# Kernel tuning notes

Hardware: AMD Instinct MI355X
Metric: run time of the kernel (lower is better)

## Reference

```python
import jax, jax.numpy as jnp
import numpy as np

D_MODEL = 1024
N_HEADS = 16
D_K = D_MODEL // N_HEADS
LN_EPS = 1e-5


def setup_inputs() -> dict:
    key = jax.random.key(0)
    ks = jax.random.split(key, 12)
    B, S, D = 4, 2048, D_MODEL
    s = 1.0 / np.sqrt(D)
    return {
        "Q": jax.random.normal(ks[0], (B, S, D), jnp.float32),
        "K": jax.random.normal(ks[1], (B, S, D), jnp.float32),
        "V": jax.random.normal(ks[2], (B, S, D), jnp.float32),
        "W_q": jax.random.normal(ks[3], (D, D), jnp.float32) * s,
        "b_q": jnp.zeros((D,), jnp.float32),
        "W_k": jax.random.normal(ks[4], (D, D), jnp.float32) * s,
        "b_k": jnp.zeros((D,), jnp.float32),
        "W_v": jax.random.normal(ks[5], (D, D), jnp.float32) * s,
        "b_v": jnp.zeros((D,), jnp.float32),
        "W_o": jax.random.normal(ks[6], (D, D), jnp.float32) * s,
        "b_o": jnp.zeros((D,), jnp.float32),
        "ln_gamma": jnp.ones((D,), jnp.float32),
        "ln_beta": jnp.zeros((D,), jnp.float32),
    }


def _split_heads(x):  # (B,S,D) -> (B,H,S,Dk)
    B, S, _ = x.shape
    return x.reshape(B, S, N_HEADS, D_K).transpose(0, 2, 1, 3)


def reference(Q, K, V, W_q, b_q, W_k, b_k, W_v, b_v, W_o, b_o, ln_gamma, ln_beta):
    # Linear projections (torch Linear: x @ W^T + b)
    q = Q @ W_q.T + b_q  # (B,S,D) -- also the residual in this module
    k = K @ W_k.T + b_k
    v = V @ W_v.T + b_v
    qh, kh, vh = _split_heads(q), _split_heads(k), _split_heads(v)
    scale = 1.0 / jnp.sqrt(jnp.float32(D_K))
    scores = jnp.einsum("bhqd,bhkd->bhqk", qh, kh) * scale
    attn = jax.nn.softmax(scores, axis=-1)  # dropout = identity (eval)
    ctx = jnp.einsum("bhqk,bhkd->bhqd", attn, vh)
    B, H, S, Dk = ctx.shape
    ctx = ctx.transpose(0, 2, 1, 3).reshape(B, S, H * Dk)  # (B,S,D)
    out = ctx @ W_o.T + b_o
    # residual uses projected Q (module quirk), then LayerNorm
    x = out + q
    mu = jnp.mean(x, axis=-1, keepdims=True)
    var = jnp.mean((x - mu) ** 2, axis=-1, keepdims=True)
    return (x - mu) * jax.lax.rsqrt(var + LN_EPS) * ln_gamma + ln_beta
```

## Files before the change

kernel.cpp:

```cpp
#include <hip/hip_runtime.h>
#include <hip/hip_bf16.h>
#include <stdint.h>

#define D_MODEL 1024
#define NH 16
#define DKH 64
#define NBATCH 4
#define SEQ 2048
#define NROWS (NBATCH*SEQ)

typedef __bf16 bf16;
typedef __bf16 bf16x8 __attribute__((ext_vector_type(8)));
typedef __bf16 bf16x4 __attribute__((ext_vector_type(4)));
typedef float f32x4 __attribute__((ext_vector_type(4)));

static __device__ __forceinline__ f32x4 fzero4() {
  f32x4 z; z[0] = 0.f; z[1] = 0.f; z[2] = 0.f; z[3] = 0.f; return z;
}

static __device__ __forceinline__ float fast_exp2(float x) {
  return __builtin_amdgcn_exp2f(x);
}

static __device__ __forceinline__ void gload16(const bf16* g, bf16* lds) {
  __builtin_amdgcn_global_load_lds(
      (const __attribute__((address_space(1))) uint32_t*)(uintptr_t)g,
      (__attribute__((address_space(3))) uint32_t*)(uintptr_t)lds,
      16, 0, 0);
}

__global__ __launch_bounds__(256) void cvt3(const float* __restrict__ Q,
                                            const float* __restrict__ K,
                                            const float* __restrict__ V,
                                            bf16* __restrict__ out) {
  const int per4 = NROWS * D_MODEL / 4;
  const float* s = blockIdx.y == 0 ? Q : (blockIdx.y == 1 ? K : V);
  int i = blockIdx.x * 256 + threadIdx.x;
  float4 v = ((const float4*)s)[i];
  bf16x4 o;
  o[0] = (bf16)v.x; o[1] = (bf16)v.y; o[2] = (bf16)v.z; o[3] = (bf16)v.w;
  ((bf16x4*)out)[blockIdx.y * per4 + i] = o;
}

__global__ __launch_bounds__(256) void cvt_w4(const float* __restrict__ a,
                                              const float* __restrict__ b,
                                              const float* __restrict__ c,
                                              const float* __restrict__ d,
                                              bf16* __restrict__ out) {
  const float* srcs[4] = {a, b, c, d};
  const float* s = srcs[blockIdx.y];
  int i = blockIdx.x * 256 + threadIdx.x;
  float4 v = ((const float4*)s)[i];
  bf16x4 o;
  o[0] = (bf16)v.x; o[1] = (bf16)v.y; o[2] = (bf16)v.z; o[3] = (bf16)v.w;
  ((bf16x4*)out)[blockIdx.y * (D_MODEL * D_MODEL / 4) + i] = o;
}

__global__ __launch_bounds__(256) void gemm_qkv(const bf16* __restrict__ Ain,
                                                const bf16* __restrict__ Wall,
                                                const float* __restrict__ bq,
                                                const float* __restrict__ bk,
                                                const float* __restrict__ bv,
                                                bf16* __restrict__ qbf,
                                                bf16* __restrict__ kpb,
                                                bf16* __restrict__ vtb) {
  __shared__ __align__(16) bf16 As[128 * 64];
  __shared__ __align__(16) bf16 Bs[128 * 64];
  const int orig = blockIdx.x + ((blockIdx.y + (blockIdx.z << 6)) << 3);
  const int work = ((orig & 7) * 192) + (orig >> 3);
  const int bn = work & 7;
  const int bm = (work >> 3) & 63;
  const int z = work >> 9;

  const bf16* A = Ain + (size_t)z * NROWS * D_MODEL;
  const bf16* B = Wall + (size_t)z * D_MODEL * D_MODEL;
  const float* bias = z == 0 ? bq : (z == 1 ? bk : bv);
  const int K = D_MODEL, N = D_MODEL;

  const int t = threadIdx.x, w = t >> 6, l = t & 63;
  const int wm = w >> 1, wn = w & 1;
  const int lr = l & 15, g = l >> 4;
  const int rowA0 = bm * 128, colB0 = bn * 128;

  f32x4 acc[4][4];
#pragma unroll
  for (int m = 0; m < 4; m++)
#pragma unroll
    for (int n = 0; n < 4; n++) acc[m][n] = fzero4();

  for (int k0 = 0; k0 < K; k0 += 64) {
#pragma unroll
    for (int i = 0; i < 4; i++) {
      int r = (w * 4 + i) * 8 + (l >> 3);
      int cb = ((l & 7) * 16) ^ ((r & 7) << 4);
      gload16(A + (size_t)(rowA0 + r) * K + k0 + (cb >> 1), As + (w * 4 + i) * 512);
      gload16(B + (size_t)(colB0 + r) * K + k0 + (cb >> 1), Bs + (w * 4 + i) * 512);
    }
    __syncthreads();
#pragma unroll
    for (int kk = 0; kk < 2; kk++) {
      bf16x8 av[4], bv4[4];
#pragma unroll
      for (int m = 0; m < 4; m++) {
        int row = wm * 64 + m * 16 + lr;
        int off = row * 128 + ((kk * 64 + g * 16) ^ ((row & 7) << 4));
        av[m] = *(const bf16x8*)((const char*)As + off);
      }
#pragma unroll
      for (int n = 0; n < 4; n++) {
        int row = wn * 64 + n * 16 + lr;
        int off = row * 128 + ((kk * 64 + g * 16) ^ ((row & 7) << 4));
        bv4[n] = *(const bf16x8*)((const char*)Bs + off);
      }
#pragma unroll
      for (int m = 0; m < 4; m++)
#pragma unroll
        for (int n = 0; n < 4; n++)
          acc[m][n] = __builtin_amdgcn_mfma_f32_16x16x32_bf16(av[m], bv4[n], acc[m][n], 0, 0, 0);
    }
    __syncthreads();
  }

  if (z == 2) {
#pragma unroll
    for (int n = 0; n < 4; n++) {
      int col = colB0 + wn * 64 + n * 16 + lr;
      float bc = bias[col];
      int hh = col >> 6, dh = col & 63;
#pragma unroll
      for (int m = 0; m < 4; m++) {
        int row = rowA0 + wm * 64 + m * 16 + g * 4;
        int bb = row >> 11;
        int ss = row & 2047;
        int pos = (ss & ~31) + g * 8 + (m & 1) * 4;
        bf16x4 o;
#pragma unroll
        for (int j = 0; j < 4; j++) o[j] = (bf16)(acc[m][n][j] + bc);
        *(bf16x4*)(vtb + (((size_t)(bb * NH + hh)) * DKH + dh) * SEQ + pos) = o;
      }
    }
  } else {
    bf16* Cb = z == 0 ? qbf : kpb;
    const float bscale = z == 0 ? 0.180336880111f : 1.0f;
#pragma unroll
    for (int n = 0; n < 4; n++) {
      int col = colB0 + wn * 64 + n * 16 + lr;
      float bc = bias[col];
#pragma unroll
      for (int m = 0; m < 4; m++) {
#pragma unroll
        for (int j = 0; j < 4; j++) {
          int row = rowA0 + wm * 64 + m * 16 + g * 4 + j;
          Cb[(size_t)row * N + col] = (bf16)((acc[m][n][j] + bc) * bscale);
        }
      }
    }
  }
}

__global__ __launch_bounds__(256) void gemm_o(const bf16* __restrict__ A,
                                              const bf16* __restrict__ B,
                                              const float* __restrict__ bias,
                                              float* __restrict__ Cf,
                                              int M, int N, int K) {
  __shared__ __align__(16) bf16 As[128 * 64];
  __shared__ __align__(16) bf16 Bs[128 * 64];
  const int orig = blockIdx.x + (blockIdx.y << 3);
  const int work = ((orig & 7) * 64) + (orig >> 3);
  const int bn = work & 7, bm = work >> 3;
  const int t = threadIdx.x, w = t >> 6, l = t & 63;
  const int wm = w >> 1, wn = w & 1;
  const int lr = l & 15, g = l >> 4;
  const int rowA0 = bm * 128, colB0 = bn * 128;

  f32x4 acc[4][4];
#pragma unroll
  for (int m = 0; m < 4; m++)
#pragma unroll
    for (int n = 0; n < 4; n++) acc[m][n] = fzero4();

  for (int k0 = 0; k0 < K; k0 += 64) {
#pragma unroll
    for (int i = 0; i < 4; i++) {
      int r = (w * 4 + i) * 8 + (l >> 3);
      int cb = ((l & 7) * 16) ^ ((r & 7) << 4);
      gload16(A + (size_t)(rowA0 + r) * K + k0 + (cb >> 1), As + (w * 4 + i) * 512);
      gload16(B + (size_t)(colB0 + r) * K + k0 + (cb >> 1), Bs + (w * 4 + i) * 512);
    }
    __syncthreads();
#pragma unroll
    for (int kk = 0; kk < 2; kk++) {
      bf16x8 av[4], bv4[4];
#pragma unroll
      for (int m = 0; m < 4; m++) {
        int row = wm * 64 + m * 16 + lr;
        int off = row * 128 + ((kk * 64 + g * 16) ^ ((row & 7) << 4));
        av[m] = *(const bf16x8*)((const char*)As + off);
      }
#pragma unroll
      for (int n = 0; n < 4; n++) {
        int row = wn * 64 + n * 16 + lr;
        int off = row * 128 + ((kk * 64 + g * 16) ^ ((row & 7) << 4));
        bv4[n] = *(const bf16x8*)((const char*)Bs + off);
      }
#pragma unroll
      for (int m = 0; m < 4; m++)
#pragma unroll
        for (int n = 0; n < 4; n++)
          acc[m][n] = __builtin_amdgcn_mfma_f32_16x16x32_bf16(av[m], bv4[n], acc[m][n], 0, 0, 0);
    }
    __syncthreads();
  }

#pragma unroll
  for (int n = 0; n < 4; n++) {
    int col = colB0 + wn * 64 + n * 16 + lr;
    float bc = bias[col];
#pragma unroll
    for (int m = 0; m < 4; m++) {
#pragma unroll
      for (int j = 0; j < 4; j++) {
        int row = rowA0 + wm * 64 + m * 16 + g * 4 + j;
        Cf[(size_t)row * N + col] = acc[m][n][j] + bc;
      }
    }
  }
}

__global__ __launch_bounds__(256, 4) void attn_fwd(const bf16* __restrict__ Qp,
                                                   const bf16* __restrict__ Kp,
                                                   const bf16* __restrict__ Vt,
                                                   bf16* __restrict__ Ctx) {
  __shared__ __align__(16) bf16 Ks[2][64 * 64];
  __shared__ __align__(16) bf16 Vs[2][64 * 64];
  const int bid0 = blockIdx.x;
  const int bid = ((bid0 & 7) << 7) | (bid0 >> 3);
  const int qt = bid & 15;
  const int h = (bid >> 4) & 15;
  const int b = bid >> 8;
  const int w = threadIdx.x >> 6, l = threadIdx.x & 63;
  const int lr = l & 15, g = l >> 4;
  const int q0 = qt * 128 + w * 32;

  const size_t qkBase = ((size_t)b * SEQ) * D_MODEL + h * DKH;
  const size_t vtBase = ((size_t)(b * NH + h)) * DKH * SEQ;
  const bf16* Kg = Kp + qkBase;
  const bf16* Vg = Vt + vtBase;

  const int sr = w * 8 + (l >> 3);
  const int scb = (l & 7) * 16;

  bf16x8 qf[2][2];
#pragma unroll
  for (int f = 0; f < 2; f++)
#pragma unroll
    for (int kk = 0; kk < 2; kk++)
      qf[f][kk] = *(const bf16x8*)(Qp + qkBase + (size_t)(q0 + f * 16 + lr) * D_MODEL + kk * 32 + g * 8);

  bf16x8 vone;
#pragma unroll
  for (int j = 0; j < 8; j++) vone[j] = (bf16)1.0f;

  f32x4 ctx[2][5];
#pragma unroll
  for (int f = 0; f < 2; f++)
#pragma unroll
    for (int n = 0; n < 5; n++) ctx[f][n] = fzero4();

#define STAGE(T, BUF)                                                         \
  {                                                                           \
    const int _s0 = (T) * 64;                                                 \
    _Pragma("unroll")                                                         \
    for (int i = 0; i < 2; i++) {                                             \
      int r = i * 32 + sr;                                                    \
      int cb = scb ^ ((r & 7) << 4);                                          \
      gload16(Kg + (size_t)(_s0 + r) * D_MODEL + (cb >> 1),                   \
              &Ks[BUF][i * 2048 + w * 512]);                                  \
      gload16(Vg + (size_t)r * SEQ + _s0 + (cb >> 1),                         \
              &Vs[BUF][i * 2048 + w * 512]);                                  \
    }                                                                         \
  }

  STAGE(0, 0);
  int cur = 0;
  for (int t = 0; t < SEQ / 64; ++t) {
    if (t + 1 < SEQ / 64) {
      STAGE(t + 1, cur ^ 1);
      asm volatile("s_waitcnt vmcnt(4)" ::: "memory");
    } else {
      asm volatile("s_waitcnt vmcnt(0)" ::: "memory");
    }
    __builtin_amdgcn_s_barrier();
    asm volatile("" ::: "memory");

#pragma unroll
    for (int ss = 0; ss < 2; ++ss) {
      bf16x8 ka[2][2];
#pragma unroll
      for (int hf = 0; hf < 2; hf++) {
        int row = ss * 32 + hf * 16 + lr;
#pragma unroll
        for (int kk = 0; kk < 2; kk++) {
          int off = row * 128 + ((kk * 64 + g * 16) ^ ((row & 7) << 4));
          ka[hf][kk] = *(const bf16x8*)((const char*)Ks[cur] + off);
        }
      }
      bf16x8 vb[4];
#pragma unroll
      for (int n = 0; n < 4; n++) {
        int row = n * 16 + lr;
        int off = row * 128 + ((ss * 64 + g * 16) ^ ((row & 7) << 4));
        vb[n] = *(const bf16x8*)((const char*)Vs[cur] + off);
      }

#pragma unroll
      for (int f = 0; f < 2; f++) {
        f32x4 sc[2];
        __builtin_amdgcn_s_setprio(1);
#pragma unroll
        for (int hf = 0; hf < 2; hf++) {
          f32x4 tt = fzero4();
          tt = __builtin_amdgcn_mfma_f32_16x16x32_bf16(ka[hf][0], qf[f][0], tt, 0, 0, 0);
          tt = __builtin_amdgcn_mfma_f32_16x16x32_bf16(ka[hf][1], qf[f][1], tt, 0, 0, 0);
          sc[hf] = tt;
        }
        __builtin_amdgcn_s_setprio(0);
        float p[8];
#pragma unroll
        for (int hf = 0; hf < 2; hf++)
#pragma unroll
          for (int j = 0; j < 4; j++)
            p[hf * 4 + j] = fast_exp2(sc[hf][j]);
        bf16x8 pa;
#pragma unroll
        for (int j = 0; j < 8; j++) pa[j] = (bf16)p[j];
        __builtin_amdgcn_s_setprio(1);
#pragma unroll
        for (int n = 0; n < 4; n++)
          ctx[f][n] = __builtin_amdgcn_mfma_f32_16x16x32_bf16(pa, vb[n], ctx[f][n], 0, 0, 0);
        ctx[f][4] = __builtin_amdgcn_mfma_f32_16x16x32_bf16(pa, vone, ctx[f][4], 0, 0, 0);
        __builtin_amdgcn_s_setprio(0);
      }
    }
    asm volatile("" ::: "memory");
    __builtin_amdgcn_s_barrier();
    cur ^= 1;
  }
#undef STAGE

#pragma unroll
  for (int f = 0; f < 2; f++) {
#pragma unroll
    for (int j = 0; j < 4; j++) {
      float lj = 1.0f / ctx[f][4][j];
      int s = q0 + f * 16 + g * 4 + j;
      size_t base = ((size_t)b * SEQ + s) * D_MODEL + h * DKH;
#pragma unroll
      for (int n = 0; n < 4; n++)
        Ctx[base + n * 16 + lr] = (bf16)(ctx[f][n][j] * lj);
    }
  }
}

__global__ __launch_bounds__(256) void ln_res(const float* __restrict__ O,
                                              const bf16* __restrict__ Rb,
                                              const float* __restrict__ gam,
                                              const float* __restrict__ bet,
                                              float* __restrict__ out) {
  const int row = blockIdx.x, t = threadIdx.x;
  const size_t idx = (size_t)row * 256 + t;
  const float4 o = ((const float4*)O)[idx];
  const bf16x4 rb = ((const bf16x4*)Rb)[idx];
  const float rs = 5.545177444479562f;
  float x0 = o.x + (float)rb[0] * rs, x1 = o.y + (float)rb[1] * rs;
  float x2 = o.z + (float)rb[2] * rs, x3 = o.w + (float)rb[3] * rs;
  float s = x0 + x1 + x2 + x3;
  float q = x0 * x0 + x1 * x1 + x2 * x2 + x3 * x3;
#pragma unroll
  for (int off = 32; off >= 1; off >>= 1) {
    s += __shfl_xor(s, off);
    q += __shfl_xor(q, off);
  }
  __shared__ float red[8];
  const int wid = t >> 6;
  if ((t & 63) == 0) { red[wid] = s; red[4 + wid] = q; }
  __syncthreads();
  s = red[0] + red[1] + red[2] + red[3];
  q = red[4] + red[5] + red[6] + red[7];
  const float mu = s * (1.f / 1024.f);
  const float rinv = rsqrtf(q * (1.f / 1024.f) - mu * mu + 1e-5f);
  const float4 g4 = ((const float4*)gam)[t];
  const float4 b4 = ((const float4*)bet)[t];
  float4 y;
  y.x = (x0 - mu) * rinv * g4.x + b4.x;
  y.y = (x1 - mu) * rinv * g4.y + b4.y;
  y.z = (x2 - mu) * rinv * g4.z + b4.z;
  y.w = (x3 - mu) * rinv * g4.w + b4.w;
  ((float4*)out)[idx] = y;
}

extern "C" void kernel_launch(void* const* d_in, const int* in_sizes, int n_in,
                              void* d_out, int out_size, void* d_ws, size_t ws_size,
                              hipStream_t stream) {
  const float* Q   = (const float*)d_in[0];
  const float* Kx  = (const float*)d_in[1];
  const float* V   = (const float*)d_in[2];
  const float* Wq  = (const float*)d_in[3];
  const float* bq  = (const float*)d_in[4];
  const float* Wk  = (const float*)d_in[5];
  const float* bk  = (const float*)d_in[6];
  const float* Wv  = (const float*)d_in[7];
  const float* bv  = (const float*)d_in[8];
  const float* Wo  = (const float*)d_in[9];
  const float* bo  = (const float*)d_in[10];
  const float* gam = (const float*)d_in[11];
  const float* bet = (const float*)d_in[12];
  float* out = (float*)d_out;

  char* ws = (char*)d_ws;
  const size_t MB = 1ull << 20;
  bf16* abf  = (bf16*)(ws);
  bf16* wall = (bf16*)(ws + 48 * MB);
  bf16* qbf  = (bf16*)(ws + 56 * MB);
  bf16* kpb  = (bf16*)(ws + 72 * MB);
  bf16* vtb  = (bf16*)(ws + 88 * MB);
  bf16* ctx  = (bf16*)(ws);
  float* attnout = (float*)(ws + 16 * MB);

  const int nW4 = D_MODEL * D_MODEL / 4;
  dim3 cb(256);

  cvt3<<<dim3(NROWS * D_MODEL / 4 / 256, 3), cb, 0, stream>>>(Q, Kx, V, abf);
  cvt_w4<<<dim3(nW4 / 256, 4), cb, 0, stream>>>(Wq, Wk, Wv, Wo, wall);

  gemm_qkv<<<dim3(8, 64, 3), cb, 0, stream>>>(abf, wall, bq, bk, bv, qbf, kpb, vtb);

  attn_fwd<<<NBATCH * NH * 16, cb, 0, stream>>>(qbf, kpb, vtb, ctx);

  gemm_o<<<dim3(8, 64), cb, 0, stream>>>(ctx, wall + 3ull * D_MODEL * D_MODEL, bo,
                                         attnout, NROWS, D_MODEL, D_MODEL);
  ln_res<<<NROWS, cb, 0, stream>>>(attnout, qbf, gam, bet, out);
}
```

Baseline: 209.9 us.

## Double-buffer LDS tiles in QKV and output GEMMs with async prefetch

Both bf16 GEMM kernels now keep two LDS buffers per operand and prefetch the k-tile two steps ahead with direct-to-LDS global loads. Each step waits with a partial vmcnt and a raw barrier instead of a full __syncthreads, so global loads overlap MFMA work. This doubles LDS use per block to 64KB, which can lower occupancy. It also relies on precise vmcnt counting that matches the number of loads per stage.

```diff
diff --git a/kernel.cpp b/kernel.cpp
--- a/kernel.cpp
+++ b/kernel.cpp
@@ -56,6 +56,19 @@
   ((bf16x4*)out)[blockIdx.y * (D_MODEL * D_MODEL / 4) + i] = o;
 }
 
+#define STAGE_G(K0, BUF)                                                      \
+  {                                                                           \
+    _Pragma("unroll")                                                         \
+    for (int i = 0; i < 4; i++) {                                             \
+      int r = (w * 4 + i) * 8 + (l >> 3);                                     \
+      int cb = ((l & 7) * 16) ^ ((r & 7) << 4);                               \
+      gload16(A + (size_t)(rowA0 + r) * D_MODEL + (K0) + (cb >> 1),           \
+              &As[BUF][(w * 4 + i) * 512]);                                   \
+      gload16(B + (size_t)(colB0 + r) * D_MODEL + (K0) + (cb >> 1),           \
+              &Bs[BUF][(w * 4 + i) * 512]);                                   \
+    }                                                                         \
+  }
+
 __global__ __launch_bounds__(256) void gemm_qkv(const bf16* __restrict__ Ain,
                                                 const bf16* __restrict__ Wall,
                                                 const float* __restrict__ bq,
@@ -64,8 +77,8 @@
                                                 bf16* __restrict__ qbf,
                                                 bf16* __restrict__ kpb,
                                                 bf16* __restrict__ vtb) {
-  __shared__ __align__(16) bf16 As[128 * 64];
-  __shared__ __align__(16) bf16 Bs[128 * 64];
+  __shared__ __align__(16) bf16 As[2][128 * 64];
+  __shared__ __align__(16) bf16 Bs[2][128 * 64];
   const int orig = blockIdx.x + ((blockIdx.y + (blockIdx.z << 6)) << 3);
   const int work = ((orig & 7) * 192) + (orig >> 3);
   const int bn = work & 7;
@@ -75,7 +88,7 @@
   const bf16* A = Ain + (size_t)z * NROWS * D_MODEL;
   const bf16* B = Wall + (size_t)z * D_MODEL * D_MODEL;
   const float* bias = z == 0 ? bq : (z == 1 ? bk : bv);
-  const int K = D_MODEL, N = D_MODEL;
+  const int N = D_MODEL;
 
   const int t = threadIdx.x, w = t >> 6, l = t & 63;
   const int wm = w >> 1, wn = w & 1;
@@ -88,15 +101,14 @@
 #pragma unroll
     for (int n = 0; n < 4; n++) acc[m][n] = fzero4();
 
-  for (int k0 = 0; k0 < K; k0 += 64) {
-#pragma unroll
-    for (int i = 0; i < 4; i++) {
-      int r = (w * 4 + i) * 8 + (l >> 3);
-      int cb = ((l & 7) * 16) ^ ((r & 7) << 4);
-      gload16(A + (size_t)(rowA0 + r) * K + k0 + (cb >> 1), As + (w * 4 + i) * 512);
-      gload16(B + (size_t)(colB0 + r) * K + k0 + (cb >> 1), Bs + (w * 4 + i) * 512);
-    }
-    __syncthreads();
+  STAGE_G(0, 0);
+  STAGE_G(64, 1);
+  int cur = 0;
+  for (int kt = 0; kt < 16; ++kt) {
+    if (kt < 15) asm volatile("s_waitcnt vmcnt(8)" ::: "memory");
+    else         asm volatile("s_waitcnt vmcnt(0)" ::: "memory");
+    __builtin_amdgcn_s_barrier();
+    asm volatile("" ::: "memory");
 #pragma unroll
     for (int kk = 0; kk < 2; kk++) {
       bf16x8 av[4], bv4[4];
@@ -104,13 +116,13 @@
       for (int m = 0; m < 4; m++) {
         int row = wm * 64 + m * 16 + lr;
         int off = row * 128 + ((kk * 64 + g * 16) ^ ((row & 7) << 4));
-        av[m] = *(const bf16x8*)((const char*)As + off);
+        av[m] = *(const bf16x8*)((const char*)As[cur] + off);
       }
 #pragma unroll
       for (int n = 0; n < 4; n++) {
         int row = wn * 64 + n * 16 + lr;
         int off = row * 128 + ((kk * 64 + g * 16) ^ ((row & 7) << 4));
-        bv4[n] = *(const bf16x8*)((const char*)Bs + off);
+        bv4[n] = *(const bf16x8*)((const char*)Bs[cur] + off);
       }
 #pragma unroll
       for (int m = 0; m < 4; m++)
@@ -118,7 +130,10 @@
         for (int n = 0; n < 4; n++)
           acc[m][n] = __builtin_amdgcn_mfma_f32_16x16x32_bf16(av[m], bv4[n], acc[m][n], 0, 0, 0);
     }
-    __syncthreads();
+    asm volatile("s_waitcnt lgkmcnt(0)" ::: "memory");
+    __builtin_amdgcn_s_barrier();
+    if (kt < 14) STAGE_G((kt + 2) * 64, cur);
+    cur ^= 1;
   }
 
   if (z == 2) {
@@ -161,10 +176,9 @@
 __global__ __launch_bounds__(256) void gemm_o(const bf16* __restrict__ A,
                                               const bf16* __restrict__ B,
                                               const float* __restrict__ bias,
-                                              float* __restrict__ Cf,
-                                              int M, int N, int K) {
-  __shared__ __align__(16) bf16 As[128 * 64];
-  __shared__ __align__(16) bf16 Bs[128 * 64];
+                                              float* __restrict__ Cf) {
+  __shared__ __align__(16) bf16 As[2][128 * 64];
+  __shared__ __align__(16) bf16 Bs[2][128 * 64];
   const int orig = blockIdx.x + (blockIdx.y << 3);
   const int work = ((orig & 7) * 64) + (orig >> 3);
   const int bn = work & 7, bm = work >> 3;
@@ -172,6 +186,7 @@
   const int wm = w >> 1, wn = w & 1;
   const int lr = l & 15, g = l >> 4;
   const int rowA0 = bm * 128, colB0 = bn * 128;
+  const int N = D_MODEL;
 
   f32x4 acc[4][4];
 #pragma unroll
@@ -179,15 +194,14 @@
 #pragma unroll
     for (int n = 0; n < 4; n++) acc[m][n] = fzero4();
 
-  for (int k0 = 0; k0 < K; k0 += 64) {
-#pragma unroll
-    for (int i = 0; i < 4; i++) {
-      int r = (w * 4 + i) * 8 + (l >> 3);
-      int cb = ((l & 7) * 16) ^ ((r & 7) << 4);
-      gload16(A + (size_t)(rowA0 + r) * K + k0 + (cb >> 1), As + (w * 4 + i) * 512);
-      gload16(B + (size_t)(colB0 + r) * K + k0 + (cb >> 1), Bs + (w * 4 + i) * 512);
-    }
-    __syncthreads();
+  STAGE_G(0, 0);
+  STAGE_G(64, 1);
+  int cur = 0;
+  for (int kt = 0; kt < 16; ++kt) {
+    if (kt < 15) asm volatile("s_waitcnt vmcnt(8)" ::: "memory");
+    else         asm volatile("s_waitcnt vmcnt(0)" ::: "memory");
+    __builtin_amdgcn_s_barrier();
+    asm volatile("" ::: "memory");
 #pragma unroll
     for (int kk = 0; kk < 2; kk++) {
       bf16x8 av[4], bv4[4];
@@ -195,13 +209,13 @@
       for (int m = 0; m < 4; m++) {
         int row = wm * 64 + m * 16 + lr;
         int off = row * 128 + ((kk * 64 + g * 16) ^ ((row & 7) << 4));
-        av[m] = *(const bf16x8*)((const char*)As + off);
+        av[m] = *(const bf16x8*)((const char*)As[cur] + off);
       }
 #pragma unroll
       for (int n = 0; n < 4; n++) {
         int row = wn * 64 + n * 16 + lr;
         int off = row * 128 + ((kk * 64 + g * 16) ^ ((row & 7) << 4));
-        bv4[n] = *(const bf16x8*)((const char*)Bs + off);
+        bv4[n] = *(const bf16x8*)((const char*)Bs[cur] + off);
       }
 #pragma unroll
       for (int m = 0; m < 4; m++)
@@ -209,7 +223,10 @@
         for (int n = 0; n < 4; n++)
           acc[m][n] = __builtin_amdgcn_mfma_f32_16x16x32_bf16(av[m], bv4[n], acc[m][n], 0, 0, 0);
     }
-    __syncthreads();
+    asm volatile("s_waitcnt lgkmcnt(0)" ::: "memory");
+    __builtin_amdgcn_s_barrier();
+    if (kt < 14) STAGE_G((kt + 2) * 64, cur);
+    cur ^= 1;
   }
 
 #pragma unroll
@@ -437,7 +454,6 @@
 
   attn_fwd<<<NBATCH * NH * 16, cb, 0, stream>>>(qbf, kpb, vtb, ctx);
 
-  gemm_o<<<dim3(8, 64), cb, 0, stream>>>(ctx, wall + 3ull * D_MODEL * D_MODEL, bo,
-                                         attnout, NROWS, D_MODEL, D_MODEL);
+  gemm_o<<<dim3(8, 64), cb, 0, stream>>>(ctx, wall + 3ull * D_MODEL * D_MODEL, bo, attnout);
   ln_res<<<NROWS, cb, 0, stream>>>(attnout, qbf, gam, bet, out);
 }
```

Measured after the change: 196.7 us. 1.07x faster.
